# Performance work log

Measured on AMD Instinct MI355X. Metric: run time of the kernel, lower is better.

## Reference

```python
import jax, jax.numpy as jnp
import numpy as np

BN_EPS = 1e-5

def _bn_eval(h, g, b, rm, rv):
    return (h - rm) * (g * jax.lax.rsqrt(rv + BN_EPS)) + b

def _gin_agg(x, edge_index, eps):
    # sum_{j->i} x_j  +  (1+eps)*x_i ; PyG convention: edge_index[0]=src, edge_index[1]=dst
    src, dst = edge_index[0], edge_index[1]
    agg = jax.ops.segment_sum(x[src], dst, num_segments=x.shape[0])
    return (1.0 + eps[0]) * x + agg


def setup_inputs() -> dict:
    key = jax.random.key(0)
    ks = jax.random.split(key, 24)
    N, E, Etr, F, H, C = 10000, 160000, 40000, 128, 512, 7

    def lin(k, fan_in, shape):
        bound = 1.0 / np.sqrt(fan_in)
        return jax.random.uniform(k, shape, jnp.float32, -bound, bound)

    inp = {
        "x": jax.random.normal(ks[0], (N, F), jnp.float32),
        "edge_index": jax.random.randint(ks[1], (2, E), 0, N, jnp.int64),
        "train_edge_id": jax.random.randint(ks[2], (Etr,), 0, E, jnp.int64),
        "eps1": jnp.zeros((1,), jnp.float32),
        "W1a": lin(ks[3], F, (F, H)), "b1a": lin(ks[4], F, (H,)),
        "W1b": lin(ks[5], H, (H, H)), "b1b": lin(ks[6], H, (H,)),
        "g1": jax.random.uniform(ks[7], (H,), jnp.float32, 0.5, 1.5),
        "be1": 0.1 * jax.random.normal(ks[8], (H,), jnp.float32),
        "rm1": 0.1 * jax.random.normal(ks[9], (H,), jnp.float32),
        "rv1": jax.random.uniform(ks[10], (H,), jnp.float32, 0.5, 1.5),
        "eps2": jnp.zeros((1,), jnp.float32),
        "W2a": lin(ks[11], H, (H, H)), "b2a": lin(ks[12], H, (H,)),
        "g2": jax.random.uniform(ks[13], (H,), jnp.float32, 0.5, 1.5),
        "be2": 0.1 * jax.random.normal(ks[14], (H,), jnp.float32),
        "rm2": 0.1 * jax.random.normal(ks[15], (H,), jnp.float32),
        "rv2": jax.random.uniform(ks[16], (H,), jnp.float32, 0.5, 1.5),
        "Wl": lin(ks[17], H, (H, H)), "bl": lin(ks[18], H, (H,)),
        "Wf": lin(ks[19], H, (H, C)), "bf": lin(ks[20], H, (C,)),
    }
    return inp


def reference(x, edge_index, train_edge_id, eps1, W1a, b1a, W1b, b1b, g1, be1, rm1, rv1,
              eps2, W2a, b2a, g2, be2, rm2, rv2, Wl, bl, Wf, bf):
    # GINConv 1: agg -> Linear-ReLU-Linear-ReLU-BN
    h = _gin_agg(x, edge_index, eps1)
    h = jax.nn.relu(h @ W1a + b1a)
    h = jax.nn.relu(h @ W1b + b1b)
    h = _bn_eval(h, g1, be1, rm1, rv1)
    # GINConv 2: agg -> Linear-ReLU-BN
    h = _gin_agg(h, edge_index, eps2)
    h = jax.nn.relu(h @ W2a + b2a)
    h = _bn_eval(h, g2, be2, rm2, rv2)
    # node head (dropout is identity in eval mode)
    h = jax.nn.relu(h @ Wl + bl)
    # edge-level scoring
    node_id = edge_index[:, train_edge_id]          # [2, Etr]
    e = h[node_id[0]] * h[node_id[1]]               # [Etr, H]
    return e @ Wf + bf                               # [Etr, C]
```

## Files before the change

### kernel.cpp

```cpp
#include <hip/hip_runtime.h>
#include <hip/hip_bf16.h>

#define N_NODES 10000
#define M_PAD   10112
#define F_IN    128
#define H_DIM   512
#define N_CLS   7

typedef __bf16  bf16x8  __attribute__((ext_vector_type(8)));
typedef float   f32x4   __attribute__((ext_vector_type(4)));
typedef ushort  ushort8 __attribute__((ext_vector_type(8)));

__device__ __forceinline__ ushort f2bf(float f) {
    union { float f; unsigned u; } x; x.f = f;
    unsigned r = x.u + 0x7fffu + ((x.u >> 16) & 1u);
    return (ushort)(r >> 16);
}
__device__ __forceinline__ float bf2f(ushort h) {
    union { unsigned u; float f; } x; x.u = ((unsigned)h) << 16;
    return x.f;
}

__device__ __forceinline__ void gload16(const void* g, void* l) {
    __builtin_amdgcn_global_load_lds(
        (const __attribute__((address_space(1))) void*)g,
        (__attribute__((address_space(3))) void*)l, 16, 0, 0);
}


__global__ void k_zero_i32(int* __restrict__ p, int n) {
    int i = blockIdx.x * blockDim.x + threadIdx.x;
    if (i < n) p[i] = 0;
}

__global__ void k_hist(const int* __restrict__ ei, int* __restrict__ counts, int E) {
    int e = blockIdx.x * blockDim.x + threadIdx.x;
    if (e < E) atomicAdd(&counts[ei[E + e]], 1);
}

__global__ __launch_bounds__(1024) void k_scan(const int* __restrict__ counts,
                                               int* __restrict__ offsets,
                                               int* __restrict__ cursor,
                                               int N, int E) {
    __shared__ int sm[1024];
    int t = threadIdx.x;
    int base = t * 10;
    int loc[10];
    int s = 0;
    #pragma unroll
    for (int i = 0; i < 10; ++i) {
        int idx = base + i;
        int c = (idx < N) ? counts[idx] : 0;
        loc[i] = s;
        s += c;
    }
    sm[t] = s;
    __syncthreads();
    for (int off = 1; off < 1024; off <<= 1) {
        int v = (t >= off) ? sm[t - off] : 0;
        __syncthreads();
        sm[t] += v;
        __syncthreads();
    }
    int excl = sm[t] - s;
    #pragma unroll
    for (int i = 0; i < 10; ++i) {
        int idx = base + i;
        if (idx < N) {
            int o = excl + loc[i];
            offsets[idx] = o;
            cursor[idx] = o;
        }
    }
    if (t == 0) offsets[N] = E;
}

__global__ void k_scatter(const int* __restrict__ ei, int* __restrict__ cursor,
                          int* __restrict__ csr_src, int E) {
    int e = blockIdx.x * blockDim.x + threadIdx.x;
    if (e < E) {
        int d = ei[E + e];
        int pos = atomicAdd(&cursor[d], 1);
        csr_src[pos] = ei[e];
    }
}


__global__ void k_wsplit(const float* __restrict__ W, ushort* __restrict__ Th,
                         ushort* __restrict__ Tl, int K, int N) {
    int idx = blockIdx.x * blockDim.x + threadIdx.x;
    if (idx >= K * N) return;
    int n = idx / K, k = idx % K;
    float w = W[(size_t)k * N + n];
    ushort hb = f2bf(w);
    Th[idx] = hb;
    Tl[idx] = f2bf(w - bf2f(hb));
}


__global__ __launch_bounds__(256) void k_agg_f32(
    const float* __restrict__ X, const int* __restrict__ csr,
    const int* __restrict__ offs, const float* __restrict__ eps,
    ushort* __restrict__ Oh, ushort* __restrict__ Ol) {
    const int wv = threadIdx.x >> 6, lane = threadIdx.x & 63;
    const int n = blockIdx.x * 4 + wv;
    if (n >= N_NODES) return;
    const int c0 = lane * 2;
    const int s0 = offs[n], s1 = offs[n + 1];
    float a0 = 0.f, a1 = 0.f;
    int i = s0;
    for (; i + 1 < s1; i += 2) {
        const float2 v0 = *(const float2*)(X + (size_t)csr[i] * F_IN + c0);
        const float2 v1 = *(const float2*)(X + (size_t)csr[i + 1] * F_IN + c0);
        a0 += v0.x + v1.x;
        a1 += v0.y + v1.y;
    }
    if (i < s1) {
        const float2 v = *(const float2*)(X + (size_t)csr[i] * F_IN + c0);
        a0 += v.x; a1 += v.y;
    }
    const float2 sv = *(const float2*)(X + (size_t)n * F_IN + c0);
    const float e = 1.f + eps[0];
    const float v0 = e * sv.x + a0;
    const float v1 = e * sv.y + a1;
    ushort2 oh, ol;
    oh.x = f2bf(v0); ol.x = f2bf(v0 - bf2f(oh.x));
    oh.y = f2bf(v1); ol.y = f2bf(v1 - bf2f(oh.y));
    const size_t o = (size_t)n * F_IN + c0;
    *(ushort2*)(Oh + o) = oh;
    *(ushort2*)(Ol + o) = ol;
}


__global__ __launch_bounds__(256) void k_agg_pair(
    const ushort* __restrict__ Xh, const ushort* __restrict__ Xl,
    const int* __restrict__ csr, const int* __restrict__ offs,
    const float* __restrict__ eps,
    ushort* __restrict__ Oh, ushort* __restrict__ Ol) {
    const int wv = threadIdx.x >> 6, lane = threadIdx.x & 63;
    const int n = blockIdx.x * 4 + wv;
    if (n >= N_NODES) return;
    const int c0 = lane * 8;
    const int s0 = offs[n], s1 = offs[n + 1];
    float acc[8] = {0.f, 0.f, 0.f, 0.f, 0.f, 0.f, 0.f, 0.f};
    int i = s0;
    for (; i + 1 < s1; i += 2) {
        const size_t b0 = (size_t)csr[i] * H_DIM + c0;
        const size_t b1 = (size_t)csr[i + 1] * H_DIM + c0;
        const ushort8 h0 = *(const ushort8*)(Xh + b0);
        const ushort8 l0 = *(const ushort8*)(Xl + b0);
        const ushort8 h1 = *(const ushort8*)(Xh + b1);
        const ushort8 l1 = *(const ushort8*)(Xl + b1);
        #pragma unroll
        for (int r = 0; r < 8; ++r)
            acc[r] += (bf2f(h0[r]) + bf2f(l0[r])) + (bf2f(h1[r]) + bf2f(l1[r]));
    }
    if (i < s1) {
        const size_t b = (size_t)csr[i] * H_DIM + c0;
        const ushort8 h = *(const ushort8*)(Xh + b);
        const ushort8 l = *(const ushort8*)(Xl + b);
        #pragma unroll
        for (int r = 0; r < 8; ++r) acc[r] += bf2f(h[r]) + bf2f(l[r]);
    }
    const size_t b = (size_t)n * H_DIM + c0;
    const ushort8 h = *(const ushort8*)(Xh + b);
    const ushort8 l = *(const ushort8*)(Xl + b);
    const float e = 1.f + eps[0];
    ushort8 oh, ol;
    #pragma unroll
    for (int r = 0; r < 8; ++r) {
        const float v = e * (bf2f(h[r]) + bf2f(l[r])) + acc[r];
        oh[r] = f2bf(v);
        ol[r] = f2bf(v - bf2f(oh[r]));
    }
    *(ushort8*)(Oh + b) = oh;
    *(ushort8*)(Ol + b) = ol;
}


template <int DO_BN>
__global__ __launch_bounds__(256) void k_gemm_mfma(
    const ushort* __restrict__ Ah, const ushort* __restrict__ Al,
    const ushort* __restrict__ Wh, const ushort* __restrict__ Wlo,
    const float* __restrict__ bias,
    const float* __restrict__ g, const float* __restrict__ be,
    const float* __restrict__ rm, const float* __restrict__ rv,
    ushort* __restrict__ Oh, ushort* __restrict__ Ol,
    int K, int Nout) {
    __shared__ __align__(16) ushort As_h[64][32];
    __shared__ __align__(16) ushort As_l[64][32];
    __shared__ __align__(16) ushort Bs_h[128][32];
    __shared__ __align__(16) ushort Bs_l[128][32];

    const int tid  = threadIdx.x;
    const int lane = tid & 63;
    const int wid  = tid >> 6;
    const int wm   = wid >> 1, wn = wid & 1;
    const int bm = blockIdx.x * 64, bn = blockIdx.y * 128;
    const int rsel = lane & 15;
    const int kh   = (lane >> 4) * 8;

    f32x4 acc[2][4];
    #pragma unroll
    for (int m = 0; m < 2; ++m)
        #pragma unroll
        for (int n = 0; n < 4; ++n) {
            acc[m][n][0] = 0.f; acc[m][n][1] = 0.f;
            acc[m][n][2] = 0.f; acc[m][n][3] = 0.f;
        }

    for (int k0 = 0; k0 < K; k0 += 32) {
        {
            const int off = tid * 16;
            const int row = off >> 6;
            const int ke  = (off & 63) >> 1;
            const size_t ga = (size_t)(bm + row) * K + (k0 + ke);
            gload16(Ah + ga, (char*)As_h + off);
            gload16(Al + ga, (char*)As_l + off);
        }
        #pragma unroll
        for (int c = 0; c < 2; ++c) {
            const int off = tid * 16 + c * 4096;
            const int row = off >> 6;
            const int ke  = (off & 63) >> 1;
            const size_t gb = (size_t)(bn + row) * K + (k0 + ke);
            gload16(Wh + gb,  (char*)Bs_h + off);
            gload16(Wlo + gb, (char*)Bs_l + off);
        }
        __syncthreads();
        bf16x8 a_h[2], a_l[2], b_h[4], b_l[4];
        #pragma unroll
        for (int m = 0; m < 2; ++m) {
            const int r = wm * 32 + m * 16 + rsel;
            a_h[m] = *(const bf16x8*)&As_h[r][kh];
            a_l[m] = *(const bf16x8*)&As_l[r][kh];
        }
        #pragma unroll
        for (int n = 0; n < 4; ++n) {
            const int r = wn * 64 + n * 16 + rsel;
            b_h[n] = *(const bf16x8*)&Bs_h[r][kh];
            b_l[n] = *(const bf16x8*)&Bs_l[r][kh];
        }
        #pragma unroll
        for (int m = 0; m < 2; ++m)
            #pragma unroll
            for (int n = 0; n < 4; ++n) {
                acc[m][n] = __builtin_amdgcn_mfma_f32_16x16x32_bf16(a_h[m], b_h[n], acc[m][n], 0, 0, 0);
                acc[m][n] = __builtin_amdgcn_mfma_f32_16x16x32_bf16(a_h[m], b_l[n], acc[m][n], 0, 0, 0);
                acc[m][n] = __builtin_amdgcn_mfma_f32_16x16x32_bf16(a_l[m], b_h[n], acc[m][n], 0, 0, 0);
            }
        __syncthreads();
    }

    float bs[4], sc[4], sh[4];
    int cols[4];
    #pragma unroll
    for (int n = 0; n < 4; ++n) {
        const int col = bn + wn * 64 + n * 16 + rsel;
        cols[n] = col;
        bs[n] = bias[col];
        if (DO_BN) {
            const float s = g[col] * rsqrtf(rv[col] + 1e-5f);
            sc[n] = s;
            sh[n] = be[col] - rm[col] * s;
        } else {
            sc[n] = 0.f; sh[n] = 0.f;
        }
    }
    #pragma unroll
    for (int m = 0; m < 2; ++m) {
        #pragma unroll
        for (int r = 0; r < 4; ++r) {
            const int row = bm + wm * 32 + m * 16 + (lane >> 4) * 4 + r;
            #pragma unroll
            for (int n = 0; n < 4; ++n) {
                float v = acc[m][n][r] + bs[n];
                v = fmaxf(v, 0.f);
                if (DO_BN) v = v * sc[n] + sh[n];
                const ushort hb = f2bf(v);
                const ushort lb = f2bf(v - bf2f(hb));
                const size_t o = (size_t)row * Nout + cols[n];
                Oh[o] = hb;
                Ol[o] = lb;
            }
        }
    }
}


__global__ __launch_bounds__(256) void k_edge(
    const ushort* __restrict__ hh, const ushort* __restrict__ hl,
    const int* __restrict__ ei, const int* __restrict__ tids,
    const float* __restrict__ Wf, const float* __restrict__ bf_,
    float* __restrict__ out, int Etr, int E) {
    const int lane = threadIdx.x & 63;
    const int wv   = threadIdx.x >> 6;
    float wfr[8][N_CLS];
    #pragma unroll
    for (int r = 0; r < 8; ++r)
        #pragma unroll
        for (int c = 0; c < N_CLS; ++c)
            wfr[r][c] = Wf[(lane * 8 + r) * N_CLS + c];
    float bfr[N_CLS];
    #pragma unroll
    for (int c = 0; c < N_CLS; ++c) bfr[c] = bf_[c];

    const int wid  = blockIdx.x * 4 + wv;
    const int step = gridDim.x * 4;
    for (int t = wid; t < Etr; t += step) {
        const int eid = tids[t];
        const size_t a = (size_t)ei[eid] * H_DIM + lane * 8;
        const size_t b = (size_t)ei[E + eid] * H_DIM + lane * 8;
        const ushort8 ah = *(const ushort8*)(hh + a);
        const ushort8 al = *(const ushort8*)(hl + a);
        const ushort8 bh = *(const ushort8*)(hh + b);
        const ushort8 bl = *(const ushort8*)(hl + b);
        float acc[N_CLS] = {0.f, 0.f, 0.f, 0.f, 0.f, 0.f, 0.f};
        #pragma unroll
        for (int r = 0; r < 8; ++r) {
            const float va = bf2f(ah[r]) + bf2f(al[r]);
            const float vb = bf2f(bh[r]) + bf2f(bl[r]);
            const float e = va * vb;
            #pragma unroll
            for (int c = 0; c < N_CLS; ++c) acc[c] = fmaf(e, wfr[r][c], acc[c]);
        }
        #pragma unroll
        for (int o = 32; o; o >>= 1)
            #pragma unroll
            for (int c = 0; c < N_CLS; ++c) acc[c] += __shfl_xor(acc[c], o, 64);
        if (lane == 0) {
            #pragma unroll
            for (int c = 0; c < N_CLS; ++c) out[(size_t)t * N_CLS + c] = acc[c] + bfr[c];
        }
    }
}


extern "C" void kernel_launch(void* const* d_in, const int* in_sizes, int n_in,
                              void* d_out, int out_size, void* d_ws, size_t ws_size,
                              hipStream_t stream) {
    const float* x    = (const float*)d_in[0];
    const int*   ei   = (const int*)d_in[1];
    const int*   tids = (const int*)d_in[2];
    const float* eps1 = (const float*)d_in[3];
    const float* W1a  = (const float*)d_in[4];
    const float* b1a  = (const float*)d_in[5];
    const float* W1b  = (const float*)d_in[6];
    const float* b1b  = (const float*)d_in[7];
    const float* g1p  = (const float*)d_in[8];
    const float* be1  = (const float*)d_in[9];
    const float* rm1  = (const float*)d_in[10];
    const float* rv1  = (const float*)d_in[11];
    const float* eps2 = (const float*)d_in[12];
    const float* W2a  = (const float*)d_in[13];
    const float* b2a  = (const float*)d_in[14];
    const float* g2p  = (const float*)d_in[15];
    const float* be2  = (const float*)d_in[16];
    const float* rm2  = (const float*)d_in[17];
    const float* rv2  = (const float*)d_in[18];
    const float* Wl   = (const float*)d_in[19];
    const float* bl   = (const float*)d_in[20];
    const float* Wf   = (const float*)d_in[21];
    const float* bf   = (const float*)d_in[22];
    float* out = (float*)d_out;

    const int E   = in_sizes[1] / 2;
    const int Etr = in_sizes[2];

    char* ws = (char*)d_ws;
    size_t off = 0;
    auto alloc = [&](size_t bytes) -> char* {
        char* p = ws + off;
        off += (bytes + 255) & ~(size_t)255;
        return p;
    };
    int*    counts  = (int*)alloc((size_t)N_NODES * 4);
    int*    offsets = (int*)alloc((size_t)(N_NODES + 1) * 4);
    int*    cursor  = (int*)alloc((size_t)N_NODES * 4);
    int*    csr_src = (int*)alloc((size_t)E * 4);
    ushort* h0h = (ushort*)alloc((size_t)M_PAD * F_IN * 2);
    ushort* h0l = (ushort*)alloc((size_t)M_PAD * F_IN * 2);
    ushort* Ahh = (ushort*)alloc((size_t)M_PAD * H_DIM * 2);
    ushort* Ahl = (ushort*)alloc((size_t)M_PAD * H_DIM * 2);
    ushort* Bhh = (ushort*)alloc((size_t)M_PAD * H_DIM * 2);
    ushort* Bhl = (ushort*)alloc((size_t)M_PAD * H_DIM * 2);
    ushort* wt1a_h = (ushort*)alloc((size_t)H_DIM * F_IN * 2);
    ushort* wt1a_l = (ushort*)alloc((size_t)H_DIM * F_IN * 2);
    ushort* wt1b_h = (ushort*)alloc((size_t)H_DIM * H_DIM * 2);
    ushort* wt1b_l = (ushort*)alloc((size_t)H_DIM * H_DIM * 2);
    ushort* wt2a_h = (ushort*)alloc((size_t)H_DIM * H_DIM * 2);
    ushort* wt2a_l = (ushort*)alloc((size_t)H_DIM * H_DIM * 2);
    ushort* wtl_h  = (ushort*)alloc((size_t)H_DIM * H_DIM * 2);
    ushort* wtl_l  = (ushort*)alloc((size_t)H_DIM * H_DIM * 2);
    (void)ws_size; (void)n_in; (void)out_size;

    k_zero_i32<<<(N_NODES + 255) / 256, 256, 0, stream>>>(counts, N_NODES);
    k_hist<<<(E + 255) / 256, 256, 0, stream>>>(ei, counts, E);
    k_scan<<<1, 1024, 0, stream>>>(counts, offsets, cursor, N_NODES, E);
    k_scatter<<<(E + 255) / 256, 256, 0, stream>>>(ei, cursor, csr_src, E);

    k_wsplit<<<(H_DIM * F_IN + 255) / 256, 256, 0, stream>>>(W1a, wt1a_h, wt1a_l, F_IN, H_DIM);
    k_wsplit<<<(H_DIM * H_DIM + 255) / 256, 256, 0, stream>>>(W1b, wt1b_h, wt1b_l, H_DIM, H_DIM);
    k_wsplit<<<(H_DIM * H_DIM + 255) / 256, 256, 0, stream>>>(W2a, wt2a_h, wt2a_l, H_DIM, H_DIM);
    k_wsplit<<<(H_DIM * H_DIM + 255) / 256, 256, 0, stream>>>(Wl,  wtl_h,  wtl_l,  H_DIM, H_DIM);

    k_agg_f32<<<(N_NODES + 3) / 4, 256, 0, stream>>>(x, csr_src, offsets, eps1, h0h, h0l);

    dim3 gdim(M_PAD / 64, H_DIM / 128);
    k_gemm_mfma<0><<<gdim, 256, 0, stream>>>(h0h, h0l, wt1a_h, wt1a_l, b1a,
                                             nullptr, nullptr, nullptr, nullptr,
                                             Ahh, Ahl, F_IN, H_DIM);
    k_gemm_mfma<1><<<gdim, 256, 0, stream>>>(Ahh, Ahl, wt1b_h, wt1b_l, b1b,
                                             g1p, be1, rm1, rv1,
                                             Bhh, Bhl, H_DIM, H_DIM);
    k_agg_pair<<<(N_NODES + 3) / 4, 256, 0, stream>>>(Bhh, Bhl, csr_src, offsets, eps2, Ahh, Ahl);
    k_gemm_mfma<1><<<gdim, 256, 0, stream>>>(Ahh, Ahl, wt2a_h, wt2a_l, b2a,
                                             g2p, be2, rm2, rv2,
                                             Bhh, Bhl, H_DIM, H_DIM);
    k_gemm_mfma<0><<<gdim, 256, 0, stream>>>(Bhh, Bhl, wtl_h, wtl_l, bl,
                                             nullptr, nullptr, nullptr, nullptr,
                                             Ahh, Ahl, H_DIM, H_DIM);
    k_edge<<<2048, 256, 0, stream>>>(Ahh, Ahl, ei, tids, Wf, bf, out, Etr, E);
}
```

Measured before the change: 337.5 us.

## Split second-layer aggregation into column chunks with 16 nodes per block

Restructures the layer-2 neighbor aggregation so each block handles 16 nodes over one 64-column chunk of the 512 features. The hi and lo planes are split across half-groups of 16 lanes and combined with a cross-lane shuffle. Blocks sharing a chunk touch a narrower slice of the feature matrix, aiming to improve cache locality for the random gathers and raise parallelism. The cost is more redundant loads of the CSR offsets and indices, and it relies on N_NODES being divisible by 16.

```diff
diff --git a/kernel.cpp b/kernel.cpp
--- a/kernel.cpp
+++ b/kernel.cpp
@@ -6,6 +6,8 @@
 #define F_IN    128
 #define H_DIM   512
 #define N_CLS   7
+#define NCHUNK  8
+#define CCOLS   (H_DIM / NCHUNK)
 
 typedef __bf16  bf16x8  __attribute__((ext_vector_type(8)));
 typedef float   f32x4   __attribute__((ext_vector_type(4)));
@@ -137,44 +139,42 @@
     const int* __restrict__ csr, const int* __restrict__ offs,
     const float* __restrict__ eps,
     ushort* __restrict__ Oh, ushort* __restrict__ Ol) {
-    const int wv = threadIdx.x >> 6, lane = threadIdx.x & 63;
-    const int n = blockIdx.x * 4 + wv;
-    if (n >= N_NODES) return;
-    const int c0 = lane * 8;
+    const int chunk = blockIdx.x & (NCHUNK - 1);
+    const int grp   = blockIdx.x >> 3;
+    const int tid   = threadIdx.x;
+    const int n     = grp * 16 + (tid >> 4);
+    const int sub   = tid & 15;
+    const int plane = sub >> 3;
+    const int col   = chunk * CCOLS + (sub & 7) * 8;
+    const ushort* __restrict__ X = plane ? Xl : Xh;
+
     const int s0 = offs[n], s1 = offs[n + 1];
     float acc[8] = {0.f, 0.f, 0.f, 0.f, 0.f, 0.f, 0.f, 0.f};
-    int i = s0;
-    for (; i + 1 < s1; i += 2) {
-        const size_t b0 = (size_t)csr[i] * H_DIM + c0;
-        const size_t b1 = (size_t)csr[i + 1] * H_DIM + c0;
-        const ushort8 h0 = *(const ushort8*)(Xh + b0);
-        const ushort8 l0 = *(const ushort8*)(Xl + b0);
-        const ushort8 h1 = *(const ushort8*)(Xh + b1);
-        const ushort8 l1 = *(const ushort8*)(Xl + b1);
-        #pragma unroll
-        for (int r = 0; r < 8; ++r)
-            acc[r] += (bf2f(h0[r]) + bf2f(l0[r])) + (bf2f(h1[r]) + bf2f(l1[r]));
-    }
-    if (i < s1) {
-        const size_t b = (size_t)csr[i] * H_DIM + c0;
-        const ushort8 h = *(const ushort8*)(Xh + b);
-        const ushort8 l = *(const ushort8*)(Xl + b);
-        #pragma unroll
-        for (int r = 0; r < 8; ++r) acc[r] += bf2f(h[r]) + bf2f(l[r]);
-    }
-    const size_t b = (size_t)n * H_DIM + c0;
-    const ushort8 h = *(const ushort8*)(Xh + b);
-    const ushort8 l = *(const ushort8*)(Xl + b);
-    const float e = 1.f + eps[0];
-    ushort8 oh, ol;
-    #pragma unroll
-    for (int r = 0; r < 8; ++r) {
-        const float v = e * (bf2f(h[r]) + bf2f(l[r])) + acc[r];
-        oh[r] = f2bf(v);
-        ol[r] = f2bf(v - bf2f(oh[r]));
-    }
-    *(ushort8*)(Oh + b) = oh;
-    *(ushort8*)(Ol + b) = ol;
+    for (int i = s0; i < s1; ++i) {
+        const ushort8 v = *(const ushort8*)(X + (size_t)csr[i] * H_DIM + col);
+        #pragma unroll
+        for (int r = 0; r < 8; ++r) acc[r] += bf2f(v[r]);
+    }
+    {
+        const ushort8 sv = *(const ushort8*)(X + (size_t)n * H_DIM + col);
+        const float e = 1.f + eps[0];
+        #pragma unroll
+        for (int r = 0; r < 8; ++r) acc[r] += e * bf2f(sv[r]);
+    }
+    float tot[8];
+    #pragma unroll
+    for (int r = 0; r < 8; ++r) tot[r] = acc[r] + __shfl_xor(acc[r], 8, 64);
+    if (plane == 0) {
+        ushort8 oh, ol;
+        #pragma unroll
+        for (int r = 0; r < 8; ++r) {
+            oh[r] = f2bf(tot[r]);
+            ol[r] = f2bf(tot[r] - bf2f(oh[r]));
+        }
+        const size_t o = (size_t)n * H_DIM + col;
+        *(ushort8*)(Oh + o) = oh;
+        *(ushort8*)(Ol + o) = ol;
+    }
 }
 
 
@@ -413,7 +413,7 @@
     k_gemm_mfma<1><<<gdim, 256, 0, stream>>>(Ahh, Ahl, wt1b_h, wt1b_l, b1b,
                                              g1p, be1, rm1, rv1,
                                              Bhh, Bhl, H_DIM, H_DIM);
-    k_agg_pair<<<(N_NODES + 3) / 4, 256, 0, stream>>>(Bhh, Bhl, csr_src, offsets, eps2, Ahh, Ahl);
+    k_agg_pair<<<(N_NODES / 16) * NCHUNK, 256, 0, stream>>>(Bhh, Bhl, csr_src, offsets, eps2, Ahh, Ahl);
     k_gemm_mfma<1><<<gdim, 256, 0, stream>>>(Ahh, Ahl, wt2a_h, wt2a_l, b2a,
                                              g2p, be2, rm2, rv2,
                                              Bhh, Bhl, H_DIM, H_DIM);
```

After: 326.3 us. -3.3%, faster.
